# Optimization experiments

Measured on AMD Instinct MI355X. Metric: run time of the kernel, lower is better.

Reference implementation:

```python
import jax, jax.numpy as jnp
import numpy as np
from jax.scipy.special import logsumexp

EPS = 1e-6
SINKHORN_ITERS = 8
TEMPERATURE = 1.0


def sinkhorn(logits):
    # log(clamp(t, min=eps)) / temperature, then alternating row/col log-normalization
    t = jnp.log(jnp.clip(logits, EPS)) / TEMPERATURE
    for _ in range(SINKHORN_ITERS):
        t = t - logsumexp(t, axis=-2, keepdims=True)  # over tokens n
        t = t - logsumexp(t, axis=-1, keepdims=True)  # over experts e
    return jnp.exp(t)


def setup_inputs() -> dict:
    key = jax.random.key(0)
    k1, k2, k3 = jax.random.split(key, 3)
    b, n, d, e, h = 4, 4096, 1024, 8, 1
    x = jax.random.normal(k1, (b, n, d), dtype=jnp.float32)
    gate_w = jax.random.normal(k2, (h, d, e), dtype=jnp.float32)  # to_gate_weight
    experts = jax.random.normal(k3, (e, d, d), dtype=jnp.float32) * 0.02  # expert weight tensor [e, i, o]
    return {"x": x, "gate_w": gate_w, "experts": experts}


def reference(x, gate_w, experts):
    b, n, d = x.shape
    h, _, e = gate_w.shape
    m = n // e  # tokens_per_expert

    xh = x[:, None]  # b 1 n d  (single-headed path)

    # gate logits: b h n e
    gate_logits = jnp.einsum('bhnd,hde->bhne', xh, gate_w)

    # competitive sinkhorn gates (eval mode, no gumbel noise)
    gates = sinkhorn(gate_logits)

    # topk over token dim (dim=-2) with k = tokens_per_expert
    g = jnp.swapaxes(gates, -1, -2)          # b h e n
    gv, idx = jax.lax.top_k(g, m)            # b h e m
    gate_values = jnp.swapaxes(gv, -1, -2)   # b h m e
    routed_indices = jnp.swapaxes(idx, -1, -2)  # b h m e

    # eval + competitive -> hard gates
    hard_gates = (gate_values > 0.5).astype(x.dtype)  # b h m e

    # gather routed tokens: routed[b,h,m,e,d] = x[b,h,idx[b,h,m,e],d]
    bi = jnp.arange(b)[:, None, None, None]
    hi = jnp.arange(h)[None, :, None, None]
    routed = xh[bi, hi, routed_indices]  # b h m e d

    # per-expert GEMM, vectorized over experts: experts [e,i,o] -> [e,h,i,o]
    experts4 = experts[:, None, :, :]
    out = jnp.einsum('bhmei,ehio->bhmeo', routed, experts4)  # b h m e o

    # weight by gates
    out = out * hard_gates[..., None]

    # scatter back (set semantics, as in einx set_at)
    y = jnp.zeros_like(xh).at[bi, hi, routed_indices].set(out)  # b h n d
    return y[:, 0]  # b n d
```

## Files before the change

kernel.cpp:

```cpp
#include <hip/hip_runtime.h>
#include <hip/hip_bf16.h>
#include <stdint.h>

#define BB 4
#define NN 4096
#define DD 1024
#define EE 8
#define MM 512
#define BN (BB*NN)

#define FRONT_GATE 512
#define FRONT_CONV 2048
#define SKBLK 4

typedef __bf16 bf16x8 __attribute__((ext_vector_type(8)));
typedef float  floatx4 __attribute__((ext_vector_type(4)));

typedef const __attribute__((address_space(1))) void* gptr_t;
typedef __attribute__((address_space(3))) void* lptr_t;

__device__ __forceinline__ unsigned short f2bf(float f) {
    union { float f; unsigned u; } v; v.f = f;
    unsigned r = v.u + 0x7fffu + ((v.u >> 16) & 1u);
    return (unsigned short)(r >> 16);
}

__device__ __forceinline__ float fexp2(float x) { return __builtin_amdgcn_exp2f(x); }
__device__ __forceinline__ float flog2(float x) { return __builtin_amdgcn_logf(x); }

__device__ __forceinline__ float gate_reduce8(const float acc[8], int lane) {
    float k1[4];
#pragma unroll
    for (int e = 0; e < 4; e++) {
        float a = acc[e]     + __shfl_xor(acc[e],     1, 64);
        float b = acc[e + 4] + __shfl_xor(acc[e + 4], 1, 64);
        k1[e] = (lane & 1) ? b : a;
    }
    float k2[2];
#pragma unroll
    for (int e = 0; e < 2; e++) {
        float a = k1[e]     + __shfl_xor(k1[e],     2, 64);
        float b = k1[e + 2] + __shfl_xor(k1[e + 2], 2, 64);
        k2[e] = (lane & 2) ? b : a;
    }
    float a = k2[0] + __shfl_xor(k2[0], 4, 64);
    float b = k2[1] + __shfl_xor(k2[1], 4, 64);
    float v = (lane & 4) ? b : a;
    v += __shfl_xor(v, 8, 64);
    v += __shfl_xor(v, 16, 64);
    v += __shfl_xor(v, 32, 64);
    return v;
}

__device__ __forceinline__ void col_reduce(const float part[8], float c[8],
                                           float red[8][8], float* bcm,
                                           int wave, int lane, int tid) {
    float r8 = gate_reduce8(part, lane);
    if (lane < 8) {
        int eid = ((lane & 1) << 2) | (lane & 2) | ((lane & 4) >> 2);
        red[wave][eid] = r8;
    }
    __syncthreads();
    if (tid < 8) {
        float s = 0.f;
#pragma unroll
        for (int w = 0; w < 8; w++) s += red[w][tid];
        bcm[tid] = flog2(s);
    }
    __syncthreads();
#pragma unroll
    for (int e = 0; e < 8; e++) c[e] = bcm[e];
}

#define OFF_GATES   0u
#define OFF_COUNTS  655360u
#define OFF_LISTS   655616u
#define OFF_KEYS    753920u
#define OFF_XBF     1802496u
#define OFF_EXPT    35356928u
#define WS_NEEDED   52134144u

__global__ __launch_bounds__(256, 2) void gate_kernel(const float* __restrict__ x,
                                                      const float* __restrict__ gw,
                                                      float* __restrict__ tmat,
                                                      unsigned short* __restrict__ xbf,
                                                      int* __restrict__ counts) {
    int bid = blockIdx.x;
    int tid = threadIdx.x;
    if (bid >= FRONT_GATE) {
        if (tid < 32) counts[tid] = 0;
        return;
    }
    int wave = tid >> 6, lane = tid & 63;
    float4 g0[4][4], g1[4][4];
#pragma unroll
    for (int j = 0; j < 4; j++)
#pragma unroll
        for (int r = 0; r < 4; r++) {
            const float4* p = (const float4*)(gw + (size_t)(j * 256 + lane * 4 + r) * 8);
            g0[j][r] = p[0];
            g1[j][r] = p[1];
        }
    int tok0 = (bid * 4 + wave) * 8;
    int exp_id = ((lane & 1) << 2) | (lane & 2) | ((lane & 4) >> 2);

    float4 xa[4], xc[4], na[4], nc[4];
    {
        const float4* xr = (const float4*)(x + (size_t)tok0 * DD);
#pragma unroll
        for (int j = 0; j < 4; j++) xa[j] = xr[j * 64 + lane];
#pragma unroll
        for (int j = 0; j < 4; j++) xc[j] = xr[256 + j * 64 + lane];
    }
#pragma unroll
    for (int tt = 0; tt < 8; tt += 2) {
        int tokA = tok0 + tt, tokB = tokA + 1;
        if (tt < 6) {
            const float4* xrn = (const float4*)(x + (size_t)(tokA + 2) * DD);
#pragma unroll
            for (int j = 0; j < 4; j++) na[j] = xrn[j * 64 + lane];
#pragma unroll
            for (int j = 0; j < 4; j++) nc[j] = xrn[256 + j * 64 + lane];
        }
        if (xbf) {
#pragma unroll
            for (int j = 0; j < 4; j++) {
                ushort4 o;
                o.x = f2bf(xa[j].x); o.y = f2bf(xa[j].y); o.z = f2bf(xa[j].z); o.w = f2bf(xa[j].w);
                ((ushort4*)(xbf + (size_t)tokA * DD))[j * 64 + lane] = o;
            }
#pragma unroll
            for (int j = 0; j < 4; j++) {
                ushort4 o;
                o.x = f2bf(xc[j].x); o.y = f2bf(xc[j].y); o.z = f2bf(xc[j].z); o.w = f2bf(xc[j].w);
                ((ushort4*)(xbf + (size_t)tokB * DD))[j * 64 + lane] = o;
            }
        }
        float accA[8] = {0.f, 0.f, 0.f, 0.f, 0.f, 0.f, 0.f, 0.f};
        float accB[8] = {0.f, 0.f, 0.f, 0.f, 0.f, 0.f, 0.f, 0.f};
#pragma unroll
        for (int j = 0; j < 4; j++) {
            accA[0] += xa[j].x * g0[j][0].x + xa[j].y * g0[j][1].x + xa[j].z * g0[j][2].x + xa[j].w * g0[j][3].x;
            accA[1] += xa[j].x * g0[j][0].y + xa[j].y * g0[j][1].y + xa[j].z * g0[j][2].y + xa[j].w * g0[j][3].y;
            accA[2] += xa[j].x * g0[j][0].z + xa[j].y * g0[j][1].z + xa[j].z * g0[j][2].z + xa[j].w * g0[j][3].z;
            accA[3] += xa[j].x * g0[j][0].w + xa[j].y * g0[j][1].w + xa[j].z * g0[j][2].w + xa[j].w * g0[j][3].w;
            accA[4] += xa[j].x * g1[j][0].x + xa[j].y * g1[j][1].x + xa[j].z * g1[j][2].x + xa[j].w * g1[j][3].x;
            accA[5] += xa[j].x * g1[j][0].y + xa[j].y * g1[j][1].y + xa[j].z * g1[j][2].y + xa[j].w * g1[j][3].y;
            accA[6] += xa[j].x * g1[j][0].z + xa[j].y * g1[j][1].z + xa[j].z * g1[j][2].z + xa[j].w * g1[j][3].z;
            accA[7] += xa[j].x * g1[j][0].w + xa[j].y * g1[j][1].w + xa[j].z * g1[j][2].w + xa[j].w * g1[j][3].w;
            accB[0] += xc[j].x * g0[j][0].x + xc[j].y * g0[j][1].x + xc[j].z * g0[j][2].x + xc[j].w * g0[j][3].x;
            accB[1] += xc[j].x * g0[j][0].y + xc[j].y * g0[j][1].y + xc[j].z * g0[j][2].y + xc[j].w * g0[j][3].y;
            accB[2] += xc[j].x * g0[j][0].z + xc[j].y * g0[j][1].z + xc[j].z * g0[j][2].z + xc[j].w * g0[j][3].z;
            accB[3] += xc[j].x * g0[j][0].w + xc[j].y * g0[j][1].w + xc[j].z * g0[j][2].w + xc[j].w * g0[j][3].w;
            accB[4] += xc[j].x * g1[j][0].x + xc[j].y * g1[j][1].x + xc[j].z * g1[j][2].x + xc[j].w * g1[j][3].x;
            accB[5] += xc[j].x * g1[j][0].y + xc[j].y * g1[j][1].y + xc[j].z * g1[j][2].y + xc[j].w * g1[j][3].y;
            accB[6] += xc[j].x * g1[j][0].z + xc[j].y * g1[j][1].z + xc[j].z * g1[j][2].z + xc[j].w * g1[j][3].z;
            accB[7] += xc[j].x * g1[j][0].w + xc[j].y * g1[j][1].w + xc[j].z * g1[j][2].w + xc[j].w * g1[j][3].w;
        }
        float vA = gate_reduce8(accA, lane);
        float vB = gate_reduce8(accB, lane);
        if (lane < 8) {
            tmat[(size_t)tokA * EE + exp_id] = flog2(fmaxf(vA, 1e-6f));
            tmat[(size_t)tokB * EE + exp_id] = flog2(fmaxf(vB, 1e-6f));
        }
        if (tt < 6) {
#pragma unroll
            for (int j = 0; j < 4; j++) { xa[j] = na[j]; xc[j] = nc[j]; }
        }
    }
}

__global__ __launch_bounds__(512) void sinkhorn_conv(const float* __restrict__ tmat,
                                                     unsigned long long* __restrict__ keys,
                                                     int* __restrict__ rank,
                                                     const float* __restrict__ E,
                                                     unsigned short* __restrict__ expt) {
    __shared__ float tile[64][65];
    __shared__ float red[8][8];
    __shared__ float bcm[8];
    int g = blockIdx.x;
    int tid = threadIdx.x;

    if (g >= SKBLK) {
        if (!expt) return;
        int cb = g - SKBLK;
        int e = cb >> 8, t = cb & 255;
        int k0 = (t >> 4) * 64, c0 = (t & 15) * 64;
        int r = tid >> 3, c8 = (tid & 7) * 8;
        const float* src = E + ((size_t)e * DD + k0 + r) * DD + c0 + c8;
        float4 v0 = *(const float4*)src;
        float4 v1 = *(const float4*)(src + 4);
        tile[r][c8 + 0] = v0.x; tile[r][c8 + 1] = v0.y; tile[r][c8 + 2] = v0.z; tile[r][c8 + 3] = v0.w;
        tile[r][c8 + 4] = v1.x; tile[r][c8 + 5] = v1.y; tile[r][c8 + 6] = v1.z; tile[r][c8 + 7] = v1.w;
        __syncthreads();
        int cc = tid >> 3, kk8 = (tid & 7) * 8;
        ushort4 o0, o1;
        o0.x = f2bf(tile[kk8 + 0][cc]); o0.y = f2bf(tile[kk8 + 1][cc]);
        o0.z = f2bf(tile[kk8 + 2][cc]); o0.w = f2bf(tile[kk8 + 3][cc]);
        o1.x = f2bf(tile[kk8 + 4][cc]); o1.y = f2bf(tile[kk8 + 5][cc]);
        o1.z = f2bf(tile[kk8 + 6][cc]); o1.w = f2bf(tile[kk8 + 7][cc]);
        unsigned short* dst = expt + ((size_t)e * DD + c0 + cc) * DD + k0 + kk8;
        *(ushort4*)dst = o0;
        *(ushort4*)(dst + 4) = o1;
        return;
    }

    int b = g;
    int wave = tid >> 6, lane = tid & 63;
    const float* tb = tmat + (size_t)b * NN * EE;
    float c[8];

    {
        float part[8];
#pragma unroll
        for (int e = 0; e < 8; e++) part[e] = 0.f;
#pragma unroll
        for (int k = 0; k < 8; k++) {
            const float4* p = (const float4*)(tb + (size_t)(k * 512 + tid) * EE);
            float4 v0 = p[0], v1 = p[1];
            part[0] += fexp2(v0.x); part[1] += fexp2(v0.y);
            part[2] += fexp2(v0.z); part[3] += fexp2(v0.w);
            part[4] += fexp2(v1.x); part[5] += fexp2(v1.y);
            part[6] += fexp2(v1.z); part[7] += fexp2(v1.w);
        }
        col_reduce(part, c, red, bcm, wave, lane, tid);
    }

    for (int it = 0; it < 7; it++) {
        float part[8];
#pragma unroll
        for (int e = 0; e < 8; e++) part[e] = 0.f;
#pragma unroll
        for (int k = 0; k < 8; k++) {
            const float4* p = (const float4*)(tb + (size_t)(k * 512 + tid) * EE);
            float4 v0 = p[0], v1 = p[1];
            float w0 = fexp2(v0.x - c[0]), w1 = fexp2(v0.y - c[1]);
            float w2 = fexp2(v0.z - c[2]), w3 = fexp2(v0.w - c[3]);
            float w4 = fexp2(v1.x - c[4]), w5 = fexp2(v1.y - c[5]);
            float w6 = fexp2(v1.z - c[6]), w7 = fexp2(v1.w - c[7]);
            float s = ((w0 + w1) + (w2 + w3)) + ((w4 + w5) + (w6 + w7));
            float rk = flog2(s);
            part[0] += fexp2(v0.x - rk); part[1] += fexp2(v0.y - rk);
            part[2] += fexp2(v0.z - rk); part[3] += fexp2(v0.w - rk);
            part[4] += fexp2(v1.x - rk); part[5] += fexp2(v1.y - rk);
            part[6] += fexp2(v1.z - rk); part[7] += fexp2(v1.w - rk);
        }
        col_reduce(part, c, red, bcm, wave, lane, tid);
    }

#pragma unroll
    for (int k = 0; k < 8; k++) {
        int row = k * 512 + tid;
        const float4* p = (const float4*)(tb + (size_t)row * EE);
        float4 v0 = p[0], v1 = p[1];
        float w0 = fexp2(v0.x - c[0]), w1 = fexp2(v0.y - c[1]);
        float w2 = fexp2(v0.z - c[2]), w3 = fexp2(v0.w - c[3]);
        float w4 = fexp2(v1.x - c[4]), w5 = fexp2(v1.y - c[5]);
        float w6 = fexp2(v1.z - c[6]), w7 = fexp2(v1.w - c[7]);
        float s = ((w0 + w1) + (w2 + w3)) + ((w4 + w5) + (w6 + w7));
        float rk = flog2(s);
        unsigned long long rl = (unsigned)(~row);
        keys[(size_t)(b * EE + 0) * NN + row] = ((unsigned long long)__float_as_uint(fexp2(v0.x - c[0] - rk)) << 32) | rl;
        keys[(size_t)(b * EE + 1) * NN + row] = ((unsigned long long)__float_as_uint(fexp2(v0.y - c[1] - rk)) << 32) | rl;
        keys[(size_t)(b * EE + 2) * NN + row] = ((unsigned long long)__float_as_uint(fexp2(v0.z - c[2] - rk)) << 32) | rl;
        keys[(size_t)(b * EE + 3) * NN + row] = ((unsigned long long)__float_as_uint(fexp2(v0.w - c[3] - rk)) << 32) | rl;
        keys[(size_t)(b * EE + 4) * NN + row] = ((unsigned long long)__float_as_uint(fexp2(v1.x - c[4] - rk)) << 32) | rl;
        keys[(size_t)(b * EE + 5) * NN + row] = ((unsigned long long)__float_as_uint(fexp2(v1.y - c[5] - rk)) << 32) | rl;
        keys[(size_t)(b * EE + 6) * NN + row] = ((unsigned long long)__float_as_uint(fexp2(v1.z - c[6] - rk)) << 32) | rl;
        keys[(size_t)(b * EE + 7) * NN + row] = ((unsigned long long)__float_as_uint(fexp2(v1.w - c[7] - rk)) << 32) | rl;
    }
    __syncthreads();
    {
        int4* rz = (int4*)(rank + (size_t)b * EE * NN);
        int4 z4 = make_int4(0, 0, 0, 0);
#pragma unroll
        for (int q = 0; q < 16; q++) rz[q * 512 + tid] = z4;
    }
}

__global__ __launch_bounds__(256) void rank_count_kernel(const unsigned long long* __restrict__ keys,
                                                         int* __restrict__ rank) {
    int be = blockIdx.y;
    int tid = threadIdx.x;
    int t = blockIdx.x * 256 + tid;
    const unsigned long long* kcol = keys + (size_t)be * NN;
    unsigned long long my = kcol[t];
    const unsigned long long* ks = kcol + (size_t)blockIdx.z * (NN / 4);

    int c0 = 0, c1 = 0, c2 = 0, c3 = 0;
    for (int j = 0; j < NN / 4; j += 16) {
#pragma unroll
        for (int i = 0; i < 16; i += 4) {
            c0 += (int)(ks[j + i + 0] > my);
            c1 += (int)(ks[j + i + 1] > my);
            c2 += (int)(ks[j + i + 2] > my);
            c3 += (int)(ks[j + i + 3] > my);
        }
    }
    atomicAdd(&rank[(size_t)be * NN + t], (c0 + c1) + (c2 + c3));
}

__global__ __launch_bounds__(256) void build_zero_kernel(const unsigned long long* __restrict__ keys,
                                                         const int* __restrict__ rank,
                                                         int* __restrict__ counts,
                                                         int* __restrict__ lists,
                                                         float* __restrict__ y) {
    __shared__ int act_s[64];
    int base = blockIdx.x * 64;
    int tid = threadIdx.x;
    if (tid < 64) {
        int i = base + tid;
        int b = i >> 12, tok = i & 4095;
        int wmax = -1;
#pragma unroll
        for (int e = 0; e < EE; e++) {
            int r = rank[(size_t)(b * 8 + e) * NN + tok];
            if (r < MM) {
                int w = r * 8 + e;
                wmax = wmax > w ? wmax : w;
            }
        }
        int active = 0;
        if (wmax >= 0) {
            int ew = wmax & 7;
            unsigned hi = (unsigned)(keys[(size_t)(b * 8 + ew) * NN + tok] >> 32);
            if (__uint_as_float(hi) > 0.5f) {
                int p = atomicAdd(&counts[b * 8 + ew], 1);
                lists[(b * 8 + ew) * MM + p] = tok;
                active = 1;
            }
        }
        act_s[tid] = active;
    }
    __syncthreads();
    float4 z = make_float4(0.f, 0.f, 0.f, 0.f);
    for (int r = 0; r < 64; r++) {
        if (!act_s[r])
            ((float4*)(y + (size_t)(base + r) * DD))[tid] = z;
    }
}

__global__ __launch_bounds__(256) void expert_gemm_mfma(const unsigned short* __restrict__ xbf,
                                                        const unsigned short* __restrict__ expt,
                                                        const int* __restrict__ counts,
                                                        const int* __restrict__ lists,
                                                        float* __restrict__ y) {
    int be = blockIdx.z;
    int b = be >> 3, e = be & 7;
    int cnt = counts[be];
    int row0 = blockIdx.y * 64;
    if (row0 >= cnt) return;
    int col0 = blockIdx.x * 128;

    __shared__ unsigned short As[64 * 32];
    __shared__ unsigned short Bs[128 * 32];
    __shared__ int toks[64];

    int tid = threadIdx.x;
    int wave = tid >> 6, lane = tid & 63;
    int m16 = lane & 15, quad = lane >> 4;
    int wave_m = wave >> 1, wave_n = wave & 1;

    if (tid < 64) {
        int r = row0 + tid;
        toks[tid] = lists[be * MM + (r < cnt ? r : cnt - 1)];
    }

    int r0 = tid >> 2;
    int ch = tid & 3;

    const unsigned short* xb = xbf + (size_t)b * NN * DD;
    const unsigned short* Eb = expt + (size_t)e * DD * DD;

    floatx4 acc[2][4];
#pragma unroll
    for (int i = 0; i < 2; i++)
#pragma unroll
        for (int j = 0; j < 4; j++) acc[i][j] = (floatx4)0.f;

    for (int k0 = 0; k0 < DD; k0 += 32) {
        __syncthreads();
        {
            const unsigned short* gA  = xb + (size_t)toks[r0] * DD + k0 + ch * 8;
            const unsigned short* gB0 = Eb + (size_t)(col0 + r0) * DD + k0 + ch * 8;
            const unsigned short* gB1 = Eb + (size_t)(col0 + 64 + r0) * DD + k0 + ch * 8;
            __builtin_amdgcn_global_load_lds((gptr_t)gA,  (lptr_t)(As + (size_t)tid * 8), 16, 0, 0);
            __builtin_amdgcn_global_load_lds((gptr_t)gB0, (lptr_t)(Bs + (size_t)tid * 8), 16, 0, 0);
            __builtin_amdgcn_global_load_lds((gptr_t)gB1, (lptr_t)(Bs + 64 * 32 + (size_t)tid * 8), 16, 0, 0);
        }
        __syncthreads();
        bf16x8 af[2], bfr[4];
#pragma unroll
        for (int i = 0; i < 2; i++)
            af[i] = *(const bf16x8*)&As[(wave_m * 32 + i * 16 + m16) * 32 + quad * 8];
#pragma unroll
        for (int j = 0; j < 4; j++)
            bfr[j] = *(const bf16x8*)&Bs[(wave_n * 64 + j * 16 + m16) * 32 + quad * 8];
#pragma unroll
        for (int i = 0; i < 2; i++)
#pragma unroll
            for (int j = 0; j < 4; j++)
                acc[i][j] = __builtin_amdgcn_mfma_f32_16x16x32_bf16(af[i], bfr[j], acc[i][j], 0, 0, 0);
    }

#pragma unroll
    for (int i = 0; i < 2; i++) {
#pragma unroll
        for (int r = 0; r < 4; r++) {
            int lr = wave_m * 32 + i * 16 + quad * 4 + r;
            if (row0 + lr < cnt) {
                int tok = toks[lr];
                float* yr = y + ((size_t)b * NN + tok) * DD + col0 + wave_n * 64 + m16;
#pragma unroll
                for (int j = 0; j < 4; j++) yr[j * 16] = acc[i][j][r];
            }
        }
    }
}

__global__ __launch_bounds__(256) void expert_gemm_kernel(const float* __restrict__ x,
                                                          const float* __restrict__ experts,
                                                          const int* __restrict__ counts,
                                                          const int* __restrict__ lists,
                                                          float* __restrict__ y) {
    int be = blockIdx.z;
    int b = be >> 3, e = be & 7;
    int cnt = counts[be];
    int row0 = blockIdx.y * 64;
    if (row0 >= cnt) return;
    int col0 = blockIdx.x * 64;
    __shared__ float As2[16][68];
    __shared__ float Bs2[16][68];
    __shared__ int toks[64];
    int tid = threadIdx.x;
    if (tid < 64) {
        int r = row0 + tid;
        toks[tid] = (r < cnt) ? lists[be * MM + r] : -1;
    }
    __syncthreads();
    int tx = tid & 15, ty = tid >> 4;
    int ar = tid >> 2;
    int ak = (tid & 3) * 4;
    int bk = tid >> 4;
    int bc4 = (tid & 15) * 4;
    int atok = toks[ar];
    const float* xb = x + (size_t)b * NN * DD;
    const float* Eb = experts + (size_t)e * DD * DD + col0;
    float acc[4][4] = {};
    for (int k0 = 0; k0 < DD; k0 += 16) {
        float4 av;
        if (atok >= 0) av = *(const float4*)(xb + (size_t)atok * DD + k0 + ak);
        else av = make_float4(0.f, 0.f, 0.f, 0.f);
        float4 bv = *(const float4*)(Eb + (size_t)(k0 + bk) * DD + bc4);
        __syncthreads();
        As2[ak + 0][ar] = av.x; As2[ak + 1][ar] = av.y; As2[ak + 2][ar] = av.z; As2[ak + 3][ar] = av.w;
        *(float4*)&Bs2[bk][bc4] = bv;
        __syncthreads();
#pragma unroll
        for (int kk = 0; kk < 16; kk++) {
            float4 a = *(const float4*)&As2[kk][ty * 4];
            float4 bb = *(const float4*)&Bs2[kk][tx * 4];
            acc[0][0] += a.x * bb.x; acc[0][1] += a.x * bb.y; acc[0][2] += a.x * bb.z; acc[0][3] += a.x * bb.w;
            acc[1][0] += a.y * bb.x; acc[1][1] += a.y * bb.y; acc[1][2] += a.y * bb.z; acc[1][3] += a.y * bb.w;
            acc[2][0] += a.z * bb.x; acc[2][1] += a.z * bb.y; acc[2][2] += a.z * bb.z; acc[2][3] += a.z * bb.w;
            acc[3][0] += a.w * bb.x; acc[3][1] += a.w * bb.y; acc[3][2] += a.w * bb.z; acc[3][3] += a.w * bb.w;
        }
    }
#pragma unroll
    for (int i = 0; i < 4; i++) {
        int rl = ty * 4 + i;
        if (row0 + rl < cnt) {
            int tok = toks[rl];
            float4 o = make_float4(acc[i][0], acc[i][1], acc[i][2], acc[i][3]);
            *(float4*)(y + ((size_t)b * NN + tok) * DD + col0 + tx * 4) = o;
        }
    }
}

extern "C" void kernel_launch(void* const* d_in, const int* in_sizes, int n_in,
                              void* d_out, int out_size, void* d_ws, size_t ws_size,
                              hipStream_t stream) {
    const float* x       = (const float*)d_in[0];
    const float* gw      = (const float*)d_in[1];
    const float* experts = (const float*)d_in[2];
    float* y = (float*)d_out;

    char* ws = (char*)d_ws;
    float*    gates    = (float*)(ws + OFF_GATES);
    int*      rank     = (int*)(ws + OFF_GATES);
    int*      counts   = (int*)(ws + OFF_COUNTS);
    int*      lists    = (int*)(ws + OFF_LISTS);
    unsigned long long* keys = (unsigned long long*)(ws + OFF_KEYS);
    bool big = ws_size >= WS_NEEDED;
    unsigned short* xbf  = big ? (unsigned short*)(ws + OFF_XBF)  : nullptr;
    unsigned short* expt = big ? (unsigned short*)(ws + OFF_EXPT) : nullptr;

    gate_kernel<<<FRONT_GATE + 1, 256, 0, stream>>>(x, gw, gates, xbf, counts);
    sinkhorn_conv<<<SKBLK + FRONT_CONV, 512, 0, stream>>>(gates, keys, rank,
                                                          experts, expt);
    rank_count_kernel<<<dim3(16, 32, 4), 256, 0, stream>>>(keys, rank);
    build_zero_kernel<<<256, 256, 0, stream>>>(keys, rank, counts, lists, y);
    if (big)
        expert_gemm_mfma<<<dim3(8, 8, BB * EE), 256, 0, stream>>>(xbf, expt, counts, lists, y);
    else
        expert_gemm_kernel<<<dim3(16, 8, BB * EE), 256, 0, stream>>>(x, experts, counts, lists, y);
}
```

Measured before the change: 257.7 us.

## Rewrite rank counting with wave ballots over register-resident keys

```diff
diff --git a/kernel.cpp b/kernel.cpp
--- a/kernel.cpp
+++ b/kernel.cpp
@@ -12,6 +12,7 @@
 #define FRONT_GATE 512
 #define FRONT_CONV 2048
 #define SKBLK 4
+#define TCH 256
 
 typedef __bf16 bf16x8 __attribute__((ext_vector_type(8)));
 typedef float  floatx4 __attribute__((ext_vector_type(4)));
@@ -172,7 +173,6 @@
 
 __global__ __launch_bounds__(512) void sinkhorn_conv(const float* __restrict__ tmat,
                                                      unsigned long long* __restrict__ keys,
-                                                     int* __restrict__ rank,
                                                      const float* __restrict__ E,
                                                      unsigned short* __restrict__ expt) {
     __shared__ float tile[64][65];
@@ -269,35 +269,56 @@
         keys[(size_t)(b * EE + 6) * NN + row] = ((unsigned long long)__float_as_uint(fexp2(v1.z - c[6] - rk)) << 32) | rl;
         keys[(size_t)(b * EE + 7) * NN + row] = ((unsigned long long)__float_as_uint(fexp2(v1.w - c[7] - rk)) << 32) | rl;
     }
-    __syncthreads();
-    {
-        int4* rz = (int4*)(rank + (size_t)b * EE * NN);
-        int4 z4 = make_int4(0, 0, 0, 0);
-#pragma unroll
-        for (int q = 0; q < 16; q++) rz[q * 512 + tid] = z4;
-    }
-}
-
-__global__ __launch_bounds__(256) void rank_count_kernel(const unsigned long long* __restrict__ keys,
+}
+
+__global__ __launch_bounds__(512) void rank_count_kernel(const unsigned long long* __restrict__ keys,
                                                          int* __restrict__ rank) {
+    __shared__ int cnt_s[8][TCH];
     int be = blockIdx.y;
     int tid = threadIdx.x;
-    int t = blockIdx.x * 256 + tid;
+    int wave = tid >> 6, lane = tid & 63;
     const unsigned long long* kcol = keys + (size_t)be * NN;
-    unsigned long long my = kcol[t];
-    const unsigned long long* ks = kcol + (size_t)blockIdx.z * (NN / 4);
-
-    int c0 = 0, c1 = 0, c2 = 0, c3 = 0;
-    for (int j = 0; j < NN / 4; j += 16) {
-#pragma unroll
-        for (int i = 0; i < 16; i += 4) {
-            c0 += (int)(ks[j + i + 0] > my);
-            c1 += (int)(ks[j + i + 1] > my);
-            c2 += (int)(ks[j + i + 2] > my);
-            c3 += (int)(ks[j + i + 3] > my);
-        }
-    }
-    atomicAdd(&rank[(size_t)be * NN + t], (c0 + c1) + (c2 + c3));
+
+    ulonglong2 kv[4];
+    {
+        const ulonglong2* kp = (const ulonglong2*)(kcol + (size_t)wave * 512 + (size_t)lane * 8);
+#pragma unroll
+        for (int q = 0; q < 4; q++) kv[q] = kp[q];
+    }
+
+    const unsigned long long* tkp = kcol + (size_t)blockIdx.x * TCH;
+    unsigned long long tb[8], tn[8];
+#pragma unroll
+    for (int i = 0; i < 8; i++) tb[i] = tkp[i];
+
+    for (int g = 0; g < TCH / 8; g++) {
+        if (g + 1 < TCH / 8) {
+#pragma unroll
+            for (int i = 0; i < 8; i++) tn[i] = tkp[(g + 1) * 8 + i];
+        }
+#pragma unroll
+        for (int i = 0; i < 8; i++) {
+            unsigned long long tok = tb[i];
+            int cnt = 0;
+#pragma unroll
+            for (int q = 0; q < 4; q++) {
+                cnt += (int)__popcll(__ballot(kv[q].x > tok));
+                cnt += (int)__popcll(__ballot(kv[q].y > tok));
+            }
+            if (lane == 0) cnt_s[wave][g * 8 + i] = cnt;
+        }
+        if (g + 1 < TCH / 8) {
+#pragma unroll
+            for (int i = 0; i < 8; i++) tb[i] = tn[i];
+        }
+    }
+    __syncthreads();
+    if (tid < TCH) {
+        int s = 0;
+#pragma unroll
+        for (int w = 0; w < 8; w++) s += cnt_s[w][tid];
+        rank[(size_t)be * NN + blockIdx.x * TCH + tid] = s;
+    }
 }
 
 __global__ __launch_bounds__(256) void build_zero_kernel(const unsigned long long* __restrict__ keys,
@@ -496,9 +517,8 @@
     unsigned short* expt = big ? (unsigned short*)(ws + OFF_EXPT) : nullptr;
 
     gate_kernel<<<FRONT_GATE + 1, 256, 0, stream>>>(x, gw, gates, xbf, counts);
-    sinkhorn_conv<<<SKBLK + FRONT_CONV, 512, 0, stream>>>(gates, keys, rank,
-                                                          experts, expt);
-    rank_count_kernel<<<dim3(16, 32, 4), 256, 0, stream>>>(keys, rank);
+    sinkhorn_conv<<<SKBLK + FRONT_CONV, 512, 0, stream>>>(gates, keys, experts, expt);
+    rank_count_kernel<<<dim3(NN / TCH, 32), 512, 0, stream>>>(keys, rank);
     build_zero_kernel<<<256, 256, 0, stream>>>(keys, rank, counts, lists, y);
     if (big)
         expert_gemm_mfma<<<dim3(8, 8, BB * EE), 256, 0, stream>>>(xbf, expt, counts, lists, y);
```

Result: no change. 259.6 us (+0.8%).

## Reduce rank counts in shared memory instead of global atomics and zeroing

Applied to the files above, without the earlier changes.

```diff
diff --git a/kernel.cpp b/kernel.cpp
--- a/kernel.cpp
+++ b/kernel.cpp
@@ -172,7 +172,6 @@
 
 __global__ __launch_bounds__(512) void sinkhorn_conv(const float* __restrict__ tmat,
                                                      unsigned long long* __restrict__ keys,
-                                                     int* __restrict__ rank,
                                                      const float* __restrict__ E,
                                                      unsigned short* __restrict__ expt) {
     __shared__ float tile[64][65];
@@ -269,35 +268,49 @@
         keys[(size_t)(b * EE + 6) * NN + row] = ((unsigned long long)__float_as_uint(fexp2(v1.z - c[6] - rk)) << 32) | rl;
         keys[(size_t)(b * EE + 7) * NN + row] = ((unsigned long long)__float_as_uint(fexp2(v1.w - c[7] - rk)) << 32) | rl;
     }
-    __syncthreads();
-    {
-        int4* rz = (int4*)(rank + (size_t)b * EE * NN);
-        int4 z4 = make_int4(0, 0, 0, 0);
-#pragma unroll
-        for (int q = 0; q < 16; q++) rz[q * 512 + tid] = z4;
-    }
-}
-
-__global__ __launch_bounds__(256) void rank_count_kernel(const unsigned long long* __restrict__ keys,
+}
+
+__global__ __launch_bounds__(512) void rank_count_kernel(const unsigned long long* __restrict__ keys,
                                                          int* __restrict__ rank) {
+    __shared__ int cnt_s[8][64];
     int be = blockIdx.y;
     int tid = threadIdx.x;
-    int t = blockIdx.x * 256 + tid;
+    int wave = tid >> 6, lane = tid & 63;
     const unsigned long long* kcol = keys + (size_t)be * NN;
-    unsigned long long my = kcol[t];
-    const unsigned long long* ks = kcol + (size_t)blockIdx.z * (NN / 4);
+
+    unsigned long long my = kcol[blockIdx.x * 64 + lane];
+    const unsigned long long* ks = kcol + (size_t)wave * 512;
+
+    unsigned long long kb[16], kn[16];
+#pragma unroll
+    for (int i = 0; i < 16; i++) kb[i] = ks[i];
 
     int c0 = 0, c1 = 0, c2 = 0, c3 = 0;
-    for (int j = 0; j < NN / 4; j += 16) {
+    for (int j = 0; j < 512; j += 16) {
+        if (j + 16 < 512) {
+#pragma unroll
+            for (int i = 0; i < 16; i++) kn[i] = ks[j + 16 + i];
+        }
 #pragma unroll
         for (int i = 0; i < 16; i += 4) {
-            c0 += (int)(ks[j + i + 0] > my);
-            c1 += (int)(ks[j + i + 1] > my);
-            c2 += (int)(ks[j + i + 2] > my);
-            c3 += (int)(ks[j + i + 3] > my);
-        }
-    }
-    atomicAdd(&rank[(size_t)be * NN + t], (c0 + c1) + (c2 + c3));
+            c0 += (int)(kb[i + 0] > my);
+            c1 += (int)(kb[i + 1] > my);
+            c2 += (int)(kb[i + 2] > my);
+            c3 += (int)(kb[i + 3] > my);
+        }
+        if (j + 16 < 512) {
+#pragma unroll
+            for (int i = 0; i < 16; i++) kb[i] = kn[i];
+        }
+    }
+    cnt_s[wave][lane] = (c0 + c1) + (c2 + c3);
+    __syncthreads();
+    if (tid < 64) {
+        int s = 0;
+#pragma unroll
+        for (int w = 0; w < 8; w++) s += cnt_s[w][tid];
+        rank[(size_t)be * NN + blockIdx.x * 64 + tid] = s;
+    }
 }
 
 __global__ __launch_bounds__(256) void build_zero_kernel(const unsigned long long* __restrict__ keys,
@@ -496,9 +509,8 @@
     unsigned short* expt = big ? (unsigned short*)(ws + OFF_EXPT) : nullptr;
 
     gate_kernel<<<FRONT_GATE + 1, 256, 0, stream>>>(x, gw, gates, xbf, counts);
-    sinkhorn_conv<<<SKBLK + FRONT_CONV, 512, 0, stream>>>(gates, keys, rank,
-                                                          experts, expt);
-    rank_count_kernel<<<dim3(16, 32, 4), 256, 0, stream>>>(keys, rank);
+    sinkhorn_conv<<<SKBLK + FRONT_CONV, 512, 0, stream>>>(gates, keys, experts, expt);
+    rank_count_kernel<<<dim3(NN / 64, 32), 512, 0, stream>>>(keys, rank);
     build_zero_kernel<<<256, 256, 0, stream>>>(keys, rank, counts, lists, y);
     if (big)
         expert_gemm_mfma<<<dim3(8, 8, BB * EE), 256, 0, stream>>>(xbf, expt, counts, lists, y);
```

Result: slower. 335.6 us (+30.2%).
